# Performance work log

Measured on AMD Instinct MI355X. Metric: run time of the kernel, lower is better.

The kernel has to match this reference:

```python
import jax, jax.numpy as jnp
import numpy as np

BATCH, N_GRAPHS, N_NODES, UNITS = 512, 3, 4096, 256

def setup_inputs() -> dict:
    key = jax.random.key(0)
    ks = jax.random.split(key, 11)
    return {
        "inputs": jax.random.normal(ks[0], (BATCH, N_NODES), jnp.float32),
        "state": jax.random.normal(ks[1], (BATCH, UNITS), jnp.float32),
        "adj": jax.random.uniform(ks[2], (N_GRAPHS, N_NODES, N_NODES), jnp.float32),
        "wa": jax.random.uniform(ks[3], (N_GRAPHS,), jnp.float32),
        "w_gcn": jax.random.normal(ks[4], (N_NODES, UNITS), jnp.float32) * (1.0 / np.sqrt(N_NODES)),
        "wz": jax.random.normal(ks[5], (UNITS, UNITS), jnp.float32) * 0.05,
        "uz": jax.random.normal(ks[6], (UNITS, UNITS), jnp.float32) * 0.05,
        "bz": jax.random.normal(ks[7], (UNITS,), jnp.float32) * 0.05,
        "wh": jax.random.normal(ks[8], (UNITS, UNITS), jnp.float32) * 0.05,
        "uh": jax.random.normal(ks[9], (UNITS, UNITS), jnp.float32) * 0.05,
        "bh": jax.random.normal(ks[10], (UNITS,), jnp.float32) * 0.05,
    }

def reference(inputs, state, adj, wa, w_gcn, wz, uz, bz, wh, uh, bh):
    # Weighted sum of the n_graphs adjacency matrices: [g],[g,n,n] -> [n,n]
    adj_mix = jnp.einsum('g,gnm->nm', wa, adj)
    # Graph conv: (inputs @ adj_mix) @ w_gcn, then ReLU -> [batch, units]
    x = jax.nn.relu(jnp.matmul(jnp.matmul(inputs, adj_mix), w_gcn))
    # GRU-style gating
    z = jax.nn.sigmoid(x @ wz + state @ uz + bz)
    h_tilde = jnp.tanh(x @ wh + state @ uh + bh)
    out = (1.0 - z) * state + z * h_tilde
    return out
```

## Files before the change

### kernel.cpp

```cpp
#include <hip/hip_runtime.h>
#include <stdint.h>

typedef _Float16 f16;
typedef __attribute__((ext_vector_type(8))) _Float16 f16x8;
typedef __attribute__((ext_vector_type(4))) float f32x4;

#define NN 4096
#define UN 256

__device__ __forceinline__ f16x8 ld_f16x8(const f16* p){ return *(const f16x8*)p; }
__device__ __forceinline__ f32x4 zero4(){ f32x4 z = {0.f,0.f,0.f,0.f}; return z; }


__global__ __launch_bounds__(256) void k0_prep(
    const float* __restrict__ wg, const float* __restrict__ wz,
    const float* __restrict__ uz, const float* __restrict__ wh,
    const float* __restrict__ uh,
    f16* __restrict__ wgB,
    f16* __restrict__ czB_h, f16* __restrict__ czB_l,
    f16* __restrict__ chB_h, f16* __restrict__ chB_l)
{
  __shared__ float lsA[32*256];
  __shared__ float lsB[32*256];
  const int t = threadIdx.x;
  const int b = blockIdx.x;
  if (b < 128){
    const int kcg = b;
    #pragma unroll 8
    for (int i = 0; i < 32; i++)
      lsA[i*256 + t] = wg[(size_t)(kcg*32 + i) * UN + t];
    __syncthreads();
    #pragma unroll
    for (int i = 0; i < 4; i++){
      int o = i*256 + t;
      int l = o & 63;
      int n = ((o >> 6) << 4) + (l & 15);
      int kl = (l >> 4) * 8;
      f16 v8[8];
      #pragma unroll
      for (int j = 0; j < 8; j++) v8[j] = (f16)lsA[(kl + j)*256 + n];
      *(uint4*)(wgB + ((size_t)kcg*1024 + o)*8) = *(const uint4*)v8;
    }
  } else {
    const int kcg = b - 128;
    #pragma unroll 8
    for (int i = 0; i < 32; i++){
      int kg = kcg*32 + i;
      lsA[i*256 + t] = (kg < 256) ? wz[(size_t)kg * UN + t]
                                  : uz[(size_t)(kg - 256) * UN + t];
      lsB[i*256 + t] = (kg < 256) ? wh[(size_t)kg * UN + t]
                                  : uh[(size_t)(kg - 256) * UN + t];
    }
    __syncthreads();
    #pragma unroll
    for (int i = 0; i < 4; i++){
      int o = i*256 + t;
      int l = o & 63;
      int n = ((o >> 6) << 4) + (l & 15);
      int kl = (l >> 4) * 8;
      f16 zh[8], zl[8], hh[8], hl[8];
      #pragma unroll
      for (int j = 0; j < 8; j++){
        float vz = lsA[(kl + j)*256 + n];
        float vh = lsB[(kl + j)*256 + n];
        f16 a = (f16)vz; zh[j] = a; zl[j] = (f16)(vz - (float)a);
        f16 c = (f16)vh; hh[j] = c; hl[j] = (f16)(vh - (float)c);
      }
      size_t off = ((size_t)kcg*1024 + o)*8;
      *(uint4*)(czB_h + off) = *(const uint4*)zh;
      *(uint4*)(czB_l + off) = *(const uint4*)zl;
      *(uint4*)(chB_h + off) = *(const uint4*)hh;
      *(uint4*)(chB_l + off) = *(const uint4*)hl;
    }
  }
}

__global__ __launch_bounds__(256) void k1_w2(
    const float* __restrict__ adj, const float* __restrict__ wa,
    const f16* __restrict__ wgB, float* __restrict__ W2)
{
  const int t = threadIdx.x, lane = t & 63, wv = t >> 6;
  const int qm = lane & 15, quad = lane >> 4;
  const int mbase = blockIdx.x * 64 + wv * 16;
  const int kbase = blockIdx.y * 256;
  const float wa0 = wa[0], wa1 = wa[1], wa2 = wa[2];
  const size_t gs = (size_t)NN * NN;
  const float* pa = adj + (size_t)(mbase + qm) * NN + kbase + quad * 8;

  f32x4 acc[16];
  #pragma unroll
  for (int i = 0; i < 16; i++) acc[i] = zero4();

  f32x4 g[6];
  #pragma unroll
  for (int r = 0; r < 2; r++)
    #pragma unroll
    for (int gi = 0; gi < 3; gi++)
      g[gi*2 + r] = *(const f32x4*)(pa + (size_t)gi*gs + r*4);

  for (int step = 0; step < 8; step++){
    const int kc = step * 32;
    const int kcg = (kbase + kc) >> 5;
    const f16* pb = wgB + ((size_t)kcg*1024 + lane)*8;

    f16x8 bf[8];
    #pragma unroll
    for (int i = 0; i < 8; i++) bf[i] = ld_f16x8(pb + i*512);

    f16x8 ah, al;
    #pragma unroll
    for (int j = 0; j < 4; j++){
      float v0 = wa0*g[0][j] + wa1*g[2][j] + wa2*g[4][j];
      float v1 = wa0*g[1][j] + wa1*g[3][j] + wa2*g[5][j];
      f16 h0 = (f16)v0, h1 = (f16)v1;
      ah[j] = h0;   al[j] = (f16)(v0 - (float)h0);
      ah[4+j] = h1; al[4+j] = (f16)(v1 - (float)h1);
    }

    f32x4 gn[6];
    if (step < 7){
      const float* pan = pa + kc + 32;
      #pragma unroll
      for (int r = 0; r < 2; r++)
        #pragma unroll
        for (int gi = 0; gi < 3; gi++)
          gn[gi*2 + r] = *(const f32x4*)(pan + (size_t)gi*gs + r*4);
    }

    f16x8 bg[8];
    #pragma unroll
    for (int i = 0; i < 8; i++) bg[i] = ld_f16x8(pb + (8+i)*512);

    #pragma unroll
    for (int tn = 0; tn < 8; tn++){
      acc[tn] = __builtin_amdgcn_mfma_f32_16x16x32_f16(ah, bf[tn], acc[tn], 0, 0, 0);
      acc[tn] = __builtin_amdgcn_mfma_f32_16x16x32_f16(al, bf[tn], acc[tn], 0, 0, 0);
    }
    #pragma unroll
    for (int tn = 0; tn < 8; tn++){
      acc[8+tn] = __builtin_amdgcn_mfma_f32_16x16x32_f16(ah, bg[tn], acc[8+tn], 0, 0, 0);
      acc[8+tn] = __builtin_amdgcn_mfma_f32_16x16x32_f16(al, bg[tn], acc[8+tn], 0, 0, 0);
    }

    #pragma unroll
    for (int i = 0; i < 6; i++) g[i] = gn[i];
  }

  #pragma unroll
  for (int tn = 0; tn < 16; tn++)
    #pragma unroll
    for (int r = 0; r < 4; r++)
      atomicAdd(&W2[(size_t)(mbase + quad*4 + r)*UN + tn*16 + qm], acc[tn][r]);
}

__global__ __launch_bounds__(256) void k_cvt(
    const float* __restrict__ W2, f16* __restrict__ W2B)
{
  __shared__ float ls[32*256];
  const int t = threadIdx.x;
  const int kcg = blockIdx.x;
  #pragma unroll 8
  for (int i = 0; i < 32; i++)
    ls[i*256 + t] = W2[(size_t)(kcg*32 + i) * UN + t];
  __syncthreads();
  #pragma unroll
  for (int i = 0; i < 4; i++){
    int o = i*256 + t;
    int l = o & 63;
    int n = ((o >> 6) << 4) + (l & 15);
    int kl = (l >> 4) * 8;
    f16 v8[8];
    #pragma unroll
    for (int j = 0; j < 8; j++) v8[j] = (f16)ls[(kl + j)*256 + n];
    *(uint4*)(W2B + ((size_t)kcg*1024 + o)*8) = *(const uint4*)v8;
  }
}

__global__ __launch_bounds__(256) void k2_x(
    const float* __restrict__ inputs, const f16* __restrict__ W2B,
    float* __restrict__ xg)
{
  const int t = threadIdx.x, lane = t & 63, wv = t >> 6;
  const int qm = lane & 15, quad = lane >> 4;
  const int m0 = blockIdx.x * 16;
  const int kbase = blockIdx.y * 128;
  const float* pa = inputs + (size_t)(m0 + qm) * NN + kbase + quad * 8;

  f32x4 acc[4] = { zero4(), zero4(), zero4(), zero4() };

  #pragma unroll
  for (int kc = 0; kc < 128; kc += 32){
    f32x4 a0 = *(const f32x4*)(pa + kc);
    f32x4 a1 = *(const f32x4*)(pa + kc + 4);
    const int kcg = (kbase + kc) >> 5;
    const f16* pb = W2B + (((size_t)kcg*16 + wv*4)*64 + lane)*8;
    f16x8 bfr[4];
    #pragma unroll
    for (int tn = 0; tn < 4; tn++) bfr[tn] = ld_f16x8(pb + tn*512);
    f16x8 ah, al;
    #pragma unroll
    for (int j = 0; j < 4; j++){
      f16 h0 = (f16)a0[j], h1 = (f16)a1[j];
      ah[j] = h0;   al[j] = (f16)(a0[j] - (float)h0);
      ah[4+j] = h1; al[4+j] = (f16)(a1[j] - (float)h1);
    }
    #pragma unroll
    for (int tn = 0; tn < 4; tn++){
      acc[tn] = __builtin_amdgcn_mfma_f32_16x16x32_f16(ah, bfr[tn], acc[tn], 0, 0, 0);
      acc[tn] = __builtin_amdgcn_mfma_f32_16x16x32_f16(al, bfr[tn], acc[tn], 0, 0, 0);
    }
  }
  #pragma unroll
  for (int tn = 0; tn < 4; tn++)
    #pragma unroll
    for (int r = 0; r < 4; r++)
      atomicAdd(&xg[(size_t)(m0 + quad*4 + r)*UN + (wv*4 + tn)*16 + qm],
                acc[tn][r]);
}

__global__ __launch_bounds__(256) void k2b_xa(
    const float* __restrict__ xg, const float* __restrict__ state,
    f16* __restrict__ xa_h, f16* __restrict__ xa_l)
{
  const size_t e = ((size_t)blockIdx.x * 256 + threadIdx.x) * 8;
  const int m = (int)(e >> 9), k0 = (int)(e & 511);
  const float* src = (k0 < 256) ? (xg + (size_t)m * UN + k0)
                                : (state + (size_t)m * UN + (k0 - 256));
  f32x4 a = *(const f32x4*)src;
  f32x4 b = *(const f32x4*)(src + 4);
  const bool rl = (k0 < 256);
  f16 hi[8], lo[8];
  #pragma unroll
  for (int j = 0; j < 4; j++){
    float va = rl ? fmaxf(a[j], 0.f) : a[j];
    float vb = rl ? fmaxf(b[j], 0.f) : b[j];
    f16 ha = (f16)va, hb = (f16)vb;
    hi[j] = ha;   lo[j] = (f16)(va - (float)ha);
    hi[4+j] = hb; lo[4+j] = (f16)(vb - (float)hb);
  }
  *(uint4*)(xa_h + e) = *(const uint4*)hi;
  *(uint4*)(xa_l + e) = *(const uint4*)lo;
}

__global__ __launch_bounds__(256) void k3_gates(
    const f16* __restrict__ xa_h, const f16* __restrict__ xa_l,
    const f16* __restrict__ czB_h, const f16* __restrict__ czB_l,
    const f16* __restrict__ chB_h, const f16* __restrict__ chB_l,
    float* __restrict__ lz, float* __restrict__ lh)
{
  const int t = threadIdx.x, lane = t & 63, wv = t >> 6;
  const int qm = lane & 15, quad = lane >> 4;
  const int m0 = blockIdx.x * 16;
  const int kbase = blockIdx.y * 32;
  const size_t pao = (size_t)(m0 + qm) * 512 + kbase + quad * 8;

  f32x4 az[4] = { zero4(), zero4(), zero4(), zero4() };
  f32x4 ag[4] = { zero4(), zero4(), zero4(), zero4() };

  f16x8 ah = ld_f16x8(xa_h + pao);
  f16x8 al = ld_f16x8(xa_l + pao);
  const int kcg = kbase >> 5;
  const size_t base = (((size_t)kcg*16 + wv*4)*64 + lane)*8;
  #pragma unroll
  for (int tn = 0; tn < 4; tn++){
    f16x8 bzh = ld_f16x8(czB_h + base + tn*512);
    f16x8 bzl = ld_f16x8(czB_l + base + tn*512);
    f16x8 bhh = ld_f16x8(chB_h + base + tn*512);
    f16x8 bhl = ld_f16x8(chB_l + base + tn*512);
    az[tn] = __builtin_amdgcn_mfma_f32_16x16x32_f16(ah, bzh, az[tn], 0, 0, 0);
    az[tn] = __builtin_amdgcn_mfma_f32_16x16x32_f16(al, bzh, az[tn], 0, 0, 0);
    az[tn] = __builtin_amdgcn_mfma_f32_16x16x32_f16(ah, bzl, az[tn], 0, 0, 0);
    ag[tn] = __builtin_amdgcn_mfma_f32_16x16x32_f16(ah, bhh, ag[tn], 0, 0, 0);
    ag[tn] = __builtin_amdgcn_mfma_f32_16x16x32_f16(al, bhh, ag[tn], 0, 0, 0);
    ag[tn] = __builtin_amdgcn_mfma_f32_16x16x32_f16(ah, bhl, ag[tn], 0, 0, 0);
  }
  #pragma unroll
  for (int tn = 0; tn < 4; tn++)
    #pragma unroll
    for (int r = 0; r < 4; r++){
      size_t o = (size_t)(m0 + quad*4 + r)*UN + (wv*4 + tn)*16 + qm;
      atomicAdd(&lz[o], az[tn][r]);
      atomicAdd(&lh[o], ag[tn][r]);
    }
}

__global__ __launch_bounds__(256) void k3b_out(
    const float* __restrict__ lz, const float* __restrict__ lh,
    const float* __restrict__ state,
    const float* __restrict__ bz, const float* __restrict__ bh,
    float* __restrict__ out)
{
  const size_t e = ((size_t)blockIdx.x * 256 + threadIdx.x) * 4;
  const int n = (int)(e & 255);
  f32x4 z4 = *(const f32x4*)(lz + e);
  f32x4 h4 = *(const f32x4*)(lh + e);
  f32x4 s4 = *(const f32x4*)(state + e);
  f32x4 bz4 = *(const f32x4*)(bz + n);
  f32x4 bh4 = *(const f32x4*)(bh + n);
  f32x4 o4;
  #pragma unroll
  for (int j = 0; j < 4; j++){
    float z = 1.f / (1.f + __expf(-(z4[j] + bz4[j])));
    float ex = __expf(2.f * (h4[j] + bh4[j]));
    float hh = 1.f - 2.f / (ex + 1.f);
    o4[j] = (1.f - z) * s4[j] + z * hh;
  }
  *(f32x4*)(out + e) = o4;
}

extern "C" void kernel_launch(void* const* d_in, const int* in_sizes, int n_in,
                              void* d_out, int out_size, void* d_ws, size_t ws_size,
                              hipStream_t stream)
{
  const float* inputs = (const float*)d_in[0];
  const float* state  = (const float*)d_in[1];
  const float* adj    = (const float*)d_in[2];
  const float* wa     = (const float*)d_in[3];
  const float* wg     = (const float*)d_in[4];
  const float* wz     = (const float*)d_in[5];
  const float* uz     = (const float*)d_in[6];
  const float* bz     = (const float*)d_in[7];
  const float* wh     = (const float*)d_in[8];
  const float* uh     = (const float*)d_in[9];
  const float* bh     = (const float*)d_in[10];
  float* out = (float*)d_out;

  char* ws = (char*)d_ws;
  float* W2    = (float*)(ws);
  float* xg    = (float*)(ws + (4u<<20));
  float* lz    = (float*)(ws + (4u<<20) + (512u<<10));
  float* lh    = (float*)(ws + (5u<<20));
  f16* wgB     = (f16*)(ws + (5u<<20) + (512u<<10));
  f16* W2B     = (f16*)(ws + (7u<<20) + (512u<<10));
  f16* xa_h    = (f16*)(ws + (9u<<20) + (512u<<10));
  f16* xa_l    = (f16*)(ws + (10u<<20));
  f16* czB_h   = (f16*)(ws + (10u<<20) + (512u<<10));
  f16* czB_l   = (f16*)(ws + (10u<<20) + (768u<<10));
  f16* chB_h   = (f16*)(ws + (11u<<20));
  f16* chB_l   = (f16*)(ws + (11u<<20) + (256u<<10));

  hipMemsetAsync(ws, 0, (5u<<20) + (512u<<10), stream);
  k0_prep<<<144, 256, 0, stream>>>(wg, wz, uz, wh, uh,
                                   wgB, czB_h, czB_l, chB_h, chB_l);
  k1_w2<<<dim3(64, 16), 256, 0, stream>>>(adj, wa, wgB, W2);
  k_cvt<<<128, 256, 0, stream>>>(W2, W2B);
  k2_x<<<dim3(32, 32), 256, 0, stream>>>(inputs, W2B, xg);
  k2b_xa<<<128, 256, 0, stream>>>(xg, state, xa_h, xa_l);
  k3_gates<<<dim3(32, 16), 256, 0, stream>>>(xa_h, xa_l, czB_h, czB_l,
                                             chB_h, chB_l, lz, lh);
  k3b_out<<<128, 256, 0, stream>>>(lz, lh, state, bz, bh, out);
}
```

Before: 381.7 us.

## Replace split-K atomics with per-split partial buffers and reduce in consumers

Each split-K matmul kernel (W2, x, gates) now writes its partial results to a separate buffer slice with plain stores instead of float atomicAdd. The following kernels (convert, xa prep, output) sum the eight partials. The memset of the workspace is dropped and the split counts are cut, so each block does more K work. The cost is more workspace traffic, 32 MB of W2 partials that must be written and reread, plus lower grid parallelism for k1 and k2.

```diff
diff --git a/kernel.cpp b/kernel.cpp
--- a/kernel.cpp
+++ b/kernel.cpp
@@ -77,12 +77,12 @@
 
 __global__ __launch_bounds__(256) void k1_w2(
     const float* __restrict__ adj, const float* __restrict__ wa,
-    const f16* __restrict__ wgB, float* __restrict__ W2)
+    const f16* __restrict__ wgB, float* __restrict__ W2p)
 {
   const int t = threadIdx.x, lane = t & 63, wv = t >> 6;
   const int qm = lane & 15, quad = lane >> 4;
   const int mbase = blockIdx.x * 64 + wv * 16;
-  const int kbase = blockIdx.y * 256;
+  const int kbase = blockIdx.y * 512;
   const float wa0 = wa[0], wa1 = wa[1], wa2 = wa[2];
   const size_t gs = (size_t)NN * NN;
   const float* pa = adj + (size_t)(mbase + qm) * NN + kbase + quad * 8;
@@ -98,7 +98,7 @@
     for (int gi = 0; gi < 3; gi++)
       g[gi*2 + r] = *(const f32x4*)(pa + (size_t)gi*gs + r*4);
 
-  for (int step = 0; step < 8; step++){
+  for (int step = 0; step < 16; step++){
     const int kc = step * 32;
     const int kcg = (kbase + kc) >> 5;
     const f16* pb = wgB + ((size_t)kcg*1024 + lane)*8;
@@ -118,7 +118,7 @@
     }
 
     f32x4 gn[6];
-    if (step < 7){
+    if (step < 15){
       const float* pan = pa + kc + 32;
       #pragma unroll
       for (int r = 0; r < 2; r++)
@@ -146,22 +146,32 @@
     for (int i = 0; i < 6; i++) g[i] = gn[i];
   }
 
+  float* wout = W2p + (size_t)blockIdx.y * ((size_t)NN * UN);
   #pragma unroll
   for (int tn = 0; tn < 16; tn++)
     #pragma unroll
     for (int r = 0; r < 4; r++)
-      atomicAdd(&W2[(size_t)(mbase + quad*4 + r)*UN + tn*16 + qm], acc[tn][r]);
+      wout[(size_t)(mbase + quad*4 + r)*UN + tn*16 + qm] = acc[tn][r];
 }
 
 __global__ __launch_bounds__(256) void k_cvt(
-    const float* __restrict__ W2, f16* __restrict__ W2B)
+    const float* __restrict__ W2p, f16* __restrict__ W2B)
 {
   __shared__ float ls[32*256];
   const int t = threadIdx.x;
   const int kcg = blockIdx.x;
-  #pragma unroll 8
-  for (int i = 0; i < 32; i++)
-    ls[i*256 + t] = W2[(size_t)(kcg*32 + i) * UN + t];
+  const int r0 = t >> 6;
+  const int c0 = (t & 63) * 4;
+  #pragma unroll
+  for (int i = 0; i < 8; i++){
+    int r = i*4 + r0;
+    const float* src = W2p + (size_t)(kcg*32 + r) * UN + c0;
+    f32x4 s = zero4();
+    #pragma unroll
+    for (int p = 0; p < 8; p++)
+      s = s + *(const f32x4*)(src + (size_t)p * ((size_t)NN*UN));
+    *(f32x4*)(ls + r*256 + c0) = s;
+  }
   __syncthreads();
   #pragma unroll
   for (int i = 0; i < 4; i++){
@@ -178,18 +188,18 @@
 
 __global__ __launch_bounds__(256) void k2_x(
     const float* __restrict__ inputs, const f16* __restrict__ W2B,
-    float* __restrict__ xg)
+    float* __restrict__ xgp)
 {
   const int t = threadIdx.x, lane = t & 63, wv = t >> 6;
   const int qm = lane & 15, quad = lane >> 4;
   const int m0 = blockIdx.x * 16;
-  const int kbase = blockIdx.y * 128;
+  const int kbase = blockIdx.y * 512;
   const float* pa = inputs + (size_t)(m0 + qm) * NN + kbase + quad * 8;
 
   f32x4 acc[4] = { zero4(), zero4(), zero4(), zero4() };
 
-  #pragma unroll
-  for (int kc = 0; kc < 128; kc += 32){
+  #pragma unroll 4
+  for (int kc = 0; kc < 512; kc += 32){
     f32x4 a0 = *(const f32x4*)(pa + kc);
     f32x4 a1 = *(const f32x4*)(pa + kc + 4);
     const int kcg = (kbase + kc) >> 5;
@@ -210,25 +220,35 @@
       acc[tn] = __builtin_amdgcn_mfma_f32_16x16x32_f16(al, bfr[tn], acc[tn], 0, 0, 0);
     }
   }
+  float* xo = xgp + (size_t)blockIdx.y * ((size_t)512 * UN);
   #pragma unroll
   for (int tn = 0; tn < 4; tn++)
     #pragma unroll
     for (int r = 0; r < 4; r++)
-      atomicAdd(&xg[(size_t)(m0 + quad*4 + r)*UN + (wv*4 + tn)*16 + qm],
-                acc[tn][r]);
+      xo[(size_t)(m0 + quad*4 + r)*UN + (wv*4 + tn)*16 + qm] = acc[tn][r];
 }
 
 __global__ __launch_bounds__(256) void k2b_xa(
-    const float* __restrict__ xg, const float* __restrict__ state,
+    const float* __restrict__ xgp, const float* __restrict__ state,
     f16* __restrict__ xa_h, f16* __restrict__ xa_l)
 {
   const size_t e = ((size_t)blockIdx.x * 256 + threadIdx.x) * 8;
   const int m = (int)(e >> 9), k0 = (int)(e & 511);
-  const float* src = (k0 < 256) ? (xg + (size_t)m * UN + k0)
-                                : (state + (size_t)m * UN + (k0 - 256));
-  f32x4 a = *(const f32x4*)src;
-  f32x4 b = *(const f32x4*)(src + 4);
   const bool rl = (k0 < 256);
+  f32x4 a, b;
+  if (rl){
+    const float* src = xgp + (size_t)m * UN + k0;
+    a = zero4(); b = zero4();
+    #pragma unroll
+    for (int p = 0; p < 8; p++){
+      a = a + *(const f32x4*)(src + (size_t)p * (512*UN));
+      b = b + *(const f32x4*)(src + (size_t)p * (512*UN) + 4);
+    }
+  } else {
+    const float* src = state + (size_t)m * UN + (k0 - 256);
+    a = *(const f32x4*)src;
+    b = *(const f32x4*)(src + 4);
+  }
   f16 hi[8], lo[8];
   #pragma unroll
   for (int j = 0; j < 4; j++){
@@ -246,54 +266,64 @@
     const f16* __restrict__ xa_h, const f16* __restrict__ xa_l,
     const f16* __restrict__ czB_h, const f16* __restrict__ czB_l,
     const f16* __restrict__ chB_h, const f16* __restrict__ chB_l,
-    float* __restrict__ lz, float* __restrict__ lh)
+    float* __restrict__ lzp, float* __restrict__ lhp)
 {
   const int t = threadIdx.x, lane = t & 63, wv = t >> 6;
   const int qm = lane & 15, quad = lane >> 4;
   const int m0 = blockIdx.x * 16;
-  const int kbase = blockIdx.y * 32;
-  const size_t pao = (size_t)(m0 + qm) * 512 + kbase + quad * 8;
+  const int kbase = blockIdx.y * 64;
 
   f32x4 az[4] = { zero4(), zero4(), zero4(), zero4() };
   f32x4 ag[4] = { zero4(), zero4(), zero4(), zero4() };
 
-  f16x8 ah = ld_f16x8(xa_h + pao);
-  f16x8 al = ld_f16x8(xa_l + pao);
-  const int kcg = kbase >> 5;
-  const size_t base = (((size_t)kcg*16 + wv*4)*64 + lane)*8;
-  #pragma unroll
-  for (int tn = 0; tn < 4; tn++){
-    f16x8 bzh = ld_f16x8(czB_h + base + tn*512);
-    f16x8 bzl = ld_f16x8(czB_l + base + tn*512);
-    f16x8 bhh = ld_f16x8(chB_h + base + tn*512);
-    f16x8 bhl = ld_f16x8(chB_l + base + tn*512);
-    az[tn] = __builtin_amdgcn_mfma_f32_16x16x32_f16(ah, bzh, az[tn], 0, 0, 0);
-    az[tn] = __builtin_amdgcn_mfma_f32_16x16x32_f16(al, bzh, az[tn], 0, 0, 0);
-    az[tn] = __builtin_amdgcn_mfma_f32_16x16x32_f16(ah, bzl, az[tn], 0, 0, 0);
-    ag[tn] = __builtin_amdgcn_mfma_f32_16x16x32_f16(ah, bhh, ag[tn], 0, 0, 0);
-    ag[tn] = __builtin_amdgcn_mfma_f32_16x16x32_f16(al, bhh, ag[tn], 0, 0, 0);
-    ag[tn] = __builtin_amdgcn_mfma_f32_16x16x32_f16(ah, bhl, ag[tn], 0, 0, 0);
-  }
+  #pragma unroll
+  for (int kk = 0; kk < 2; kk++){
+    const int kb = kbase + kk*32;
+    const size_t pao = (size_t)(m0 + qm) * 512 + kb + quad * 8;
+    f16x8 ah = ld_f16x8(xa_h + pao);
+    f16x8 al = ld_f16x8(xa_l + pao);
+    const int kcg = kb >> 5;
+    const size_t base = (((size_t)kcg*16 + wv*4)*64 + lane)*8;
+    #pragma unroll
+    for (int tn = 0; tn < 4; tn++){
+      f16x8 bzh = ld_f16x8(czB_h + base + tn*512);
+      f16x8 bzl = ld_f16x8(czB_l + base + tn*512);
+      f16x8 bhh = ld_f16x8(chB_h + base + tn*512);
+      f16x8 bhl = ld_f16x8(chB_l + base + tn*512);
+      az[tn] = __builtin_amdgcn_mfma_f32_16x16x32_f16(ah, bzh, az[tn], 0, 0, 0);
+      az[tn] = __builtin_amdgcn_mfma_f32_16x16x32_f16(al, bzh, az[tn], 0, 0, 0);
+      az[tn] = __builtin_amdgcn_mfma_f32_16x16x32_f16(ah, bzl, az[tn], 0, 0, 0);
+      ag[tn] = __builtin_amdgcn_mfma_f32_16x16x32_f16(ah, bhh, ag[tn], 0, 0, 0);
+      ag[tn] = __builtin_amdgcn_mfma_f32_16x16x32_f16(al, bhh, ag[tn], 0, 0, 0);
+      ag[tn] = __builtin_amdgcn_mfma_f32_16x16x32_f16(ah, bhl, ag[tn], 0, 0, 0);
+    }
+  }
+  float* oz = lzp + (size_t)blockIdx.y * ((size_t)512 * UN);
+  float* oh = lhp + (size_t)blockIdx.y * ((size_t)512 * UN);
   #pragma unroll
   for (int tn = 0; tn < 4; tn++)
     #pragma unroll
     for (int r = 0; r < 4; r++){
       size_t o = (size_t)(m0 + quad*4 + r)*UN + (wv*4 + tn)*16 + qm;
-      atomicAdd(&lz[o], az[tn][r]);
-      atomicAdd(&lh[o], ag[tn][r]);
+      oz[o] = az[tn][r];
+      oh[o] = ag[tn][r];
     }
 }
 
 __global__ __launch_bounds__(256) void k3b_out(
-    const float* __restrict__ lz, const float* __restrict__ lh,
+    const float* __restrict__ lzp, const float* __restrict__ lhp,
     const float* __restrict__ state,
     const float* __restrict__ bz, const float* __restrict__ bh,
     float* __restrict__ out)
 {
   const size_t e = ((size_t)blockIdx.x * 256 + threadIdx.x) * 4;
   const int n = (int)(e & 255);
-  f32x4 z4 = *(const f32x4*)(lz + e);
-  f32x4 h4 = *(const f32x4*)(lh + e);
+  f32x4 z4 = zero4(), h4 = zero4();
+  #pragma unroll
+  for (int p = 0; p < 8; p++){
+    z4 = z4 + *(const f32x4*)(lzp + (size_t)p * (512*UN) + e);
+    h4 = h4 + *(const f32x4*)(lhp + (size_t)p * (512*UN) + e);
+  }
   f32x4 s4 = *(const f32x4*)(state + e);
   f32x4 bz4 = *(const f32x4*)(bz + n);
   f32x4 bh4 = *(const f32x4*)(bh + n);
@@ -326,27 +356,26 @@
   float* out = (float*)d_out;
 
   char* ws = (char*)d_ws;
-  float* W2    = (float*)(ws);
-  float* xg    = (float*)(ws + (4u<<20));
-  float* lz    = (float*)(ws + (4u<<20) + (512u<<10));
-  float* lh    = (float*)(ws + (5u<<20));
-  f16* wgB     = (f16*)(ws + (5u<<20) + (512u<<10));
-  f16* W2B     = (f16*)(ws + (7u<<20) + (512u<<10));
-  f16* xa_h    = (f16*)(ws + (9u<<20) + (512u<<10));
-  f16* xa_l    = (f16*)(ws + (10u<<20));
-  f16* czB_h   = (f16*)(ws + (10u<<20) + (512u<<10));
-  f16* czB_l   = (f16*)(ws + (10u<<20) + (768u<<10));
-  f16* chB_h   = (f16*)(ws + (11u<<20));
-  f16* chB_l   = (f16*)(ws + (11u<<20) + (256u<<10));
-
-  hipMemsetAsync(ws, 0, (5u<<20) + (512u<<10), stream);
+  float* W2p   = (float*)(ws);
+  float* xgp   = (float*)(ws + (32u<<20));
+  float* lzp   = (float*)(ws + (36u<<20));
+  float* lhp   = (float*)(ws + (40u<<20));
+  f16* wgB     = (f16*)(ws + (44u<<20));
+  f16* W2B     = (f16*)(ws + (46u<<20));
+  f16* xa_h    = (f16*)(ws + (48u<<20));
+  f16* xa_l    = (f16*)(ws + (48u<<20) + (512u<<10));
+  f16* czB_h   = (f16*)(ws + (49u<<20));
+  f16* czB_l   = (f16*)(ws + (49u<<20) + (256u<<10));
+  f16* chB_h   = (f16*)(ws + (49u<<20) + (512u<<10));
+  f16* chB_l   = (f16*)(ws + (49u<<20) + (768u<<10));
+
   k0_prep<<<144, 256, 0, stream>>>(wg, wz, uz, wh, uh,
                                    wgB, czB_h, czB_l, chB_h, chB_l);
-  k1_w2<<<dim3(64, 16), 256, 0, stream>>>(adj, wa, wgB, W2);
-  k_cvt<<<128, 256, 0, stream>>>(W2, W2B);
-  k2_x<<<dim3(32, 32), 256, 0, stream>>>(inputs, W2B, xg);
-  k2b_xa<<<128, 256, 0, stream>>>(xg, state, xa_h, xa_l);
-  k3_gates<<<dim3(32, 16), 256, 0, stream>>>(xa_h, xa_l, czB_h, czB_l,
-                                             chB_h, chB_l, lz, lh);
-  k3b_out<<<128, 256, 0, stream>>>(lz, lh, state, bz, bh, out);
-}
+  k1_w2<<<dim3(64, 8), 256, 0, stream>>>(adj, wa, wgB, W2p);
+  k_cvt<<<128, 256, 0, stream>>>(W2p, W2B);
+  k2_x<<<dim3(32, 8), 256, 0, stream>>>(inputs, W2B, xgp);
+  k2b_xa<<<128, 256, 0, stream>>>(xgp, state, xa_h, xa_l);
+  k3_gates<<<dim3(32, 8), 256, 0, stream>>>(xa_h, xa_l, czB_h, czB_l,
+                                            chB_h, chB_l, lzp, lhp);
+  k3b_out<<<128, 256, 0, stream>>>(lzp, lhp, state, bz, bh, out);
+}
```

Measured after the change: 347.9 us. 8.9% less time.
